# Performance work log

Hardware: AMD Instinct MI355X
Metric: run time of the kernel (lower is better)

## Reference

```python
import jax, jax.numpy as jnp
import numpy as np

TEMP = 1.0
EPS = 1e-8


def setup_inputs() -> dict:
    key = jax.random.key(0)
    k1, k2 = jax.random.split(key)
    x = jax.random.normal(k1, (8, 2048, 128), dtype=jnp.float32)
    codebook = jax.random.normal(k2, (8192, 128), dtype=jnp.float32)
    return {"x": x, "codebook": codebook}


def reference(x, codebook):
    # dim = -1: feature axis already last, moveaxis is identity.
    batch_shape = x.shape[:-1]
    xf = x.reshape(-1, x.shape[-1])  # [N, D]
    # Euclidean cdist via ||a-b||^2 = ||a||^2 + ||b||^2 - 2 a.b
    x2 = jnp.sum(xf * xf, axis=-1, keepdims=True)        # [N, 1]
    c2 = jnp.sum(codebook * codebook, axis=-1)           # [V]
    d2 = x2 + c2 - 2.0 * (xf @ codebook.T)               # [N, V]
    dists = jnp.sqrt(jnp.maximum(d2, 0.0))
    idxes = jnp.argmin(dists, axis=-1)                   # [N]
    # softmax(log(d + eps) * temp) == normalized d^temp (distance-weighted attention)
    attn = jax.nn.softmax(jnp.log(dists + EPS) * TEMP, axis=-1)  # [N, V]
    embed = attn @ codebook                              # [N, D]
    embed = embed.reshape(*batch_shape, -1)
    idxes = idxes.reshape(batch_shape)
    return embed, idxes
```

## Files before the change

### kernel.cpp

```cpp
#include <hip/hip_runtime.h>
#include <stdint.h>

#define NROWS 16384
#define DIM   128
#define VOCAB 8192
#define BN 64
#define BV 64
#define VSPLITS 4
#define SPLITV (VOCAB / VSPLITS)
#define NTILES (SPLITV / BV)
#define MARGIN  0.8f
#define EMB_ELEMS (NROWS * DIM)
#define LIST_CAP_MAX 4194304u
#define LCAP 512

typedef __attribute__((ext_vector_type(8))) short bf16x8;
typedef __attribute__((ext_vector_type(4))) float f32x4;

__device__ __forceinline__ unsigned short f2bf(float f) {
  union { float f; unsigned u; } v; v.f = f;
  unsigned r = v.u + 0x7fffu + ((v.u >> 16) & 1u);
  return (unsigned short)(r >> 16);
}

__device__ __forceinline__ int cvt_pk_bf16(float lo, float hi) {
  int r;
  asm("v_cvt_pk_bf16_f32 %0, %1, %2" : "=v"(r) : "v"(lo), "v"(hi));
  return r;
}

__device__ __forceinline__ bf16x8 pack8(float4 a, float4 b) {
  bf16x8 r;
  r[0] = (short)f2bf(a.x); r[1] = (short)f2bf(a.y);
  r[2] = (short)f2bf(a.z); r[3] = (short)f2bf(a.w);
  r[4] = (short)f2bf(b.x); r[5] = (short)f2bf(b.y);
  r[6] = (short)f2bf(b.z); r[7] = (short)f2bf(b.w);
  return r;
}

__global__ __launch_bounds__(256) void k_prep(const float* __restrict__ cb,
                                              float* __restrict__ c2,
                                              unsigned short* __restrict__ cbf) {
  int tid = threadIdx.x;
  int r = blockIdx.x * 16 + (tid >> 4);
  int l = tid & 15;
  const float* rp = cb + (size_t)r * DIM + l * 8;
  float4 a = *(const float4*)rp;
  float4 b = *(const float4*)(rp + 4);
  float s = a.x*a.x + a.y*a.y + a.z*a.z + a.w*a.w
          + b.x*b.x + b.y*b.y + b.z*b.z + b.w*b.w;
  bf16x8 v8 = pack8(a, b);
  *(bf16x8*)(cbf + (size_t)r * DIM + l * 8) = v8;
#pragma unroll
  for (int o = 1; o < 16; o <<= 1) s += __shfl_xor(s, o);
  if (l == 0) c2[r] = s;
}

__global__ __launch_bounds__(256, 4) void k_main(
    const float* __restrict__ x, const float* __restrict__ c2g,
    const unsigned short* __restrict__ cbf,
    float* __restrict__ accum,
    unsigned int* __restrict__ cnt,
    unsigned int* __restrict__ list, unsigned int cap) {
  __shared__ unsigned short tile1[BV][136];
  __shared__ unsigned short tileT[DIM][72];
  __shared__ unsigned int lbuf[LCAP];
  __shared__ unsigned int lcnt;
  __shared__ unsigned int gbase;

  const int tid = threadIdx.x;
  const int lane = tid & 63;
  const int w = tid >> 6;
  const int l15 = lane & 15, lq = lane >> 4;
  const int blockRow = blockIdx.x * BN;
  const int vy = blockIdx.y;

  if (tid == 0) lcnt = 0;

  bf16x8 afrag[4];
  float x2 = 0.f;
  {
    int gr = blockRow + w * 16 + l15;
    const float* xr = x + (size_t)gr * DIM + lq * 8;
#pragma unroll
    for (int kf = 0; kf < 4; ++kf) {
      float4 a = *(const float4*)(xr + kf * 32);
      float4 b = *(const float4*)(xr + kf * 32 + 4);
      x2 += a.x*a.x + a.y*a.y + a.z*a.z + a.w*a.w
          + b.x*b.x + b.y*b.y + b.z*b.z + b.w*b.w;
      afrag[kf] = pack8(a, b);
    }
    x2 += __shfl_xor(x2, 16);
    x2 += __shfl_xor(x2, 32);
  }

  f32x4 eacc[8];
#pragma unroll
  for (int db = 0; db < 8; ++db) eacc[db] = (f32x4){0.f, 0.f, 0.f, 0.f};
  float den = 0.f;
  float runminD = 3.0e19f;

  const int sv = (tid >> 4) * 4;
  const int sd = (tid & 15) * 8;
  const int sS = (tid & 7) << 4;

  const int srcA = (l15 + ((lane & 16) << 1)) << 2;
  const int srcB = srcA + 64;

  for (int it = 0; it < NTILES; ++it) {
    int vbase = vy * SPLITV + it * BV;
    __syncthreads();
    {
      uint4 r0 = *(const uint4*)(cbf + (size_t)(vbase + sv + 0) * DIM + sd);
      uint4 r1 = *(const uint4*)(cbf + (size_t)(vbase + sv + 1) * DIM + sd);
      uint4 r2 = *(const uint4*)(cbf + (size_t)(vbase + sv + 2) * DIM + sd);
      uint4 r3 = *(const uint4*)(cbf + (size_t)(vbase + sv + 3) * DIM + sd);
      *(uint4*)&tile1[sv + 0][sd] = r0;
      *(uint4*)&tile1[sv + 1][sd] = r1;
      *(uint4*)&tile1[sv + 2][sd] = r2;
      *(uint4*)&tile1[sv + 3][sd] = r3;
      const unsigned short* s0 = (const unsigned short*)&r0;
      const unsigned short* s1 = (const unsigned short*)&r1;
      const unsigned short* s2 = (const unsigned short*)&r2;
      const unsigned short* s3 = (const unsigned short*)&r3;
      char* tb = (char*)&tileT[0][0];
#pragma unroll
      for (int k = 0; k < 8; ++k) {
        uint2 val;
        val.x = (unsigned)s0[k] | ((unsigned)s1[k] << 16);
        val.y = (unsigned)s2[k] | ((unsigned)s3[k] << 16);
        *(uint2*)(tb + (sd + k) * 144 + ((sv * 2) ^ sS)) = val;
      }
    }
    float4 c2v0 = *(const float4*)(c2g + vbase + 0 * 16 + lq * 4);
    float4 c2v1 = *(const float4*)(c2g + vbase + 1 * 16 + lq * 4);
    float4 c2v2 = *(const float4*)(c2g + vbase + 2 * 16 + lq * 4);
    float4 c2v3 = *(const float4*)(c2g + vbase + 3 * 16 + lq * 4);
    __syncthreads();
    f32x4 sacc[4];
#pragma unroll
    for (int vi = 0; vi < 4; ++vi) sacc[vi] = (f32x4){0.f, 0.f, 0.f, 0.f};
#pragma unroll
    for (int kf = 0; kf < 4; ++kf) {
#pragma unroll
      for (int vi = 0; vi < 4; ++vi) {
        bf16x8 cf = *(const bf16x8*)&tile1[vi * 16 + l15][kf * 32 + lq * 8];
        sacc[vi] = __builtin_amdgcn_mfma_f32_16x16x32_bf16(cf, afrag[kf], sacc[vi], 0, 0, 0);
      }
    }
    float dd[4][4];
    const float* c2p[4] = {&c2v0.x, &c2v1.x, &c2v2.x, &c2v3.x};
#pragma unroll
    for (int vi = 0; vi < 4; ++vi)
#pragma unroll
      for (int j = 0; j < 4; ++j) {
        float d2 = fmaxf(fmaf(-2.f, sacc[vi][j], x2 + c2p[vi][j]), 0.f);
        float dist = sqrtf(d2) + 1e-8f;
        dd[vi][j] = dist;
        den += dist;
      }
    float rm = dd[0][0];
#pragma unroll
    for (int vi = 0; vi < 4; ++vi)
#pragma unroll
      for (int j = 0; j < 4; ++j) rm = fminf(rm, dd[vi][j]);
    rm = fminf(rm, __shfl_xor(rm, 16));
    rm = fminf(rm, __shfl_xor(rm, 32));
    runminD = fminf(runminD, rm);
    float thrD = sqrtf(fmaf(runminD, runminD, MARGIN)) + 2e-8f;
    if (__any(rm <= thrD)) {
      unsigned grow = (unsigned)(blockRow + w * 16 + l15);
#pragma unroll
      for (int vi = 0; vi < 4; ++vi)
#pragma unroll
        for (int j = 0; j < 4; ++j) {
          if (dd[vi][j] <= thrD) {
            unsigned gv = (unsigned)(vbase + vi * 16 + lq * 4 + j);
            unsigned ent = (grow << 13) | gv;
            unsigned pos = atomicAdd(&lcnt, 1u);
            if (pos < LCAP) {
              lbuf[pos] = ent;
            } else {
              unsigned gp = atomicAdd(cnt, 1u);
              if (gp < cap) list[gp] = ent;
            }
          }
        }
    }
    int wlo[4], whi[4];
#pragma unroll
    for (int vi = 0; vi < 4; ++vi) {
      wlo[vi] = cvt_pk_bf16(dd[vi][0], dd[vi][1]);
      whi[vi] = cvt_pk_bf16(dd[vi][2], dd[vi][3]);
    }
    const char* tb = (const char*)&tileT[0][0];
#pragma unroll
    for (int ks = 0; ks < 2; ++ks) {
      int v0 = ks * 2, v1 = ks * 2 + 1;
      int t0, t1;
      union { int u[4]; bf16x8 v8; } A;
      t0 = __builtin_amdgcn_ds_bpermute(srcA, wlo[v0]);
      t1 = __builtin_amdgcn_ds_bpermute(srcA, wlo[v1]);
      A.u[0] = (lq & 2) ? t1 : t0;
      t0 = __builtin_amdgcn_ds_bpermute(srcA, whi[v0]);
      t1 = __builtin_amdgcn_ds_bpermute(srcA, whi[v1]);
      A.u[1] = (lq & 2) ? t1 : t0;
      t0 = __builtin_amdgcn_ds_bpermute(srcB, wlo[v0]);
      t1 = __builtin_amdgcn_ds_bpermute(srcB, wlo[v1]);
      A.u[2] = (lq & 2) ? t1 : t0;
      t0 = __builtin_amdgcn_ds_bpermute(srcB, whi[v0]);
      t1 = __builtin_amdgcn_ds_bpermute(srcB, whi[v1]);
      A.u[3] = (lq & 2) ? t1 : t0;
      int voff = (ks * 32 + lq * 8) * 2;
#pragma unroll
      for (int db = 0; db < 8; ++db) {
        int d = db * 16 + l15;
        bf16x8 bw = *(const bf16x8*)(tb + d * 144 + (voff ^ (((d >> 3) & 7) << 4)));
        eacc[db] = __builtin_amdgcn_mfma_f32_16x16x32_bf16(A.v8, bw, eacc[db], 0, 0, 0);
      }
    }
  }
  __syncthreads();
  unsigned total = lcnt < LCAP ? lcnt : LCAP;
  if (tid == 0) gbase = atomicAdd(cnt, total);
  __syncthreads();
  for (unsigned i = tid; i < total; i += 256) {
    unsigned p = gbase + i;
    if (p < cap) list[p] = lbuf[i];
  }
#pragma unroll
  for (int db = 0; db < 8; ++db) {
#pragma unroll
    for (int j = 0; j < 4; ++j) {
      int grow = blockRow + w * 16 + lq * 4 + j;
      atomicAdd(&accum[(size_t)grow * 129 + db * 16 + l15], eacc[db][j]);
    }
  }
  den += __shfl_xor(den, 16);
  den += __shfl_xor(den, 32);
  if (lq == 0)
    atomicAdd(&accum[(size_t)(blockRow + w * 16 + l15) * 129 + 128], den);
}

__global__ __launch_bounds__(256) void k_fix(const float* __restrict__ x,
                                             const float* __restrict__ cb,
                                             const unsigned int* __restrict__ list,
                                             const unsigned int* __restrict__ cnt,
                                             unsigned int cap,
                                             unsigned long long* __restrict__ kExact) {
  unsigned n = *cnt; if (n > cap) n = cap;
  int lane = threadIdx.x & 63;
  unsigned wave = blockIdx.x * (blockDim.x >> 6) + (threadIdx.x >> 6);
  unsigned nw = gridDim.x * (blockDim.x >> 6);
  for (unsigned e = wave; e < n; e += nw) {
    unsigned ent = list[e];
    unsigned row = ent >> 13;
    unsigned v = ent & 0x1FFFu;
    const float* xr = x + (size_t)row * DIM;
    const float* cr = cb + (size_t)v * DIM;
    float2 xa = *(const float2*)(xr + lane * 2);
    float2 ca = *(const float2*)(cr + lane * 2);
    double d0 = (double)xa.x - (double)ca.x;
    double d1 = (double)xa.y - (double)ca.y;
    double acc = d0 * d0 + d1 * d1;
    for (int off = 32; off; off >>= 1) acc += __shfl_down(acc, off);
    if (lane == 0)
      atomicMin(&kExact[row],
                ((unsigned long long)__float_as_uint((float)acc) << 32) | (unsigned long long)v);
  }
}

__global__ __launch_bounds__(256) void k_rescue(const float* __restrict__ x,
                                                const float* __restrict__ cb,
                                                const unsigned int* __restrict__ cnt,
                                                unsigned int cap,
                                                unsigned long long* __restrict__ kExact) {
  if (*cnt <= cap) return;
  __shared__ float xs[4][128];
  int lane = threadIdx.x & 63;
  int wv = threadIdx.x >> 6;
  int row = blockIdx.x * 4 + wv;
  float2 xa = *(const float2*)(x + (size_t)row * DIM + lane * 2);
  xs[wv][lane * 2] = xa.x;
  xs[wv][lane * 2 + 1] = xa.y;
  __syncthreads();
  unsigned long long best = ~0ull;
  for (int v0 = 0; v0 < VOCAB; v0 += 64) {
    int v = v0 + lane;
    const float* cr = cb + (size_t)v * DIM;
    double acc = 0.0;
    for (int d = 0; d < DIM; ++d) {
      double diff = (double)xs[wv][d] - (double)cr[d];
      acc = fma(diff, diff, acc);
    }
    unsigned long long p = ((unsigned long long)__float_as_uint((float)acc) << 32)
                         | (unsigned long long)(unsigned)v;
    best = (p < best) ? p : best;
  }
#pragma unroll
  for (int off = 32; off; off >>= 1) {
    unsigned long long o = __shfl_xor(best, off);
    best = (o < best) ? o : best;
  }
  if (lane == 0) atomicMin(&kExact[row], best);
}

__global__ __launch_bounds__(256) void k_out(const float* __restrict__ accum,
                                             const unsigned long long* __restrict__ kExact,
                                             float* __restrict__ out) {
  int i = blockIdx.x * 256 + threadIdx.x;
  if (i < EMB_ELEMS) {
    int row = i >> 7, d = i & 127;
    float s = accum[(size_t)row * 129 + 128];
    out[i] = accum[(size_t)row * 129 + d] / s;
  } else {
    int n = i - EMB_ELEMS;
    out[EMB_ELEMS + n] = (float)(unsigned)(kExact[n] & 0x1FFFu);
  }
}

extern "C" void kernel_launch(void* const* d_in, const int* in_sizes, int n_in,
                              void* d_out, int out_size, void* d_ws, size_t ws_size,
                              hipStream_t stream) {
  const float* x = (const float*)d_in[0];
  const float* cb = (const float*)d_in[1];
  float* out = (float*)d_out;

  char* ws = (char*)d_ws;
  size_t off = 0;
  float* accum = (float*)(ws + off); off += (size_t)NROWS * 129 * 4;
  float* c2 = (float*)(ws + off); off += (size_t)VOCAB * 4;
  unsigned short* cbf = (unsigned short*)(ws + off); off += (size_t)VOCAB * DIM * 2;
  unsigned long long* kExact = (unsigned long long*)(ws + off); off += (size_t)NROWS * 8;
  unsigned int* cnt = (unsigned int*)(ws + off); off += 64;
  unsigned int* list = (unsigned int*)(ws + off);
  size_t cap32 = (ws_size > off) ? (ws_size - off) / 4 : 0;
  unsigned cap = (unsigned)(cap32 > LIST_CAP_MAX ? LIST_CAP_MAX : cap32);

  hipMemsetAsync(accum, 0, (size_t)NROWS * 129 * 4, stream);
  hipMemsetAsync(kExact, 0xFF, (size_t)NROWS * 8, stream);
  hipMemsetAsync(cnt, 0, 64, stream);

  k_prep<<<VOCAB / 16, 256, 0, stream>>>(cb, c2, cbf);
  k_main<<<dim3(NROWS / BN, VSPLITS), 256, 0, stream>>>(x, c2, cbf, accum, cnt, list, cap);
  k_fix<<<1024, 256, 0, stream>>>(x, cb, list, cnt, cap, kExact);
  k_rescue<<<NROWS / 4, 256, 0, stream>>>(x, cb, cnt, cap, kExact);
  k_out<<<(EMB_ELEMS + NROWS) / 256, 256, 0, stream>>>(accum, kExact, out);
}
```

Baseline: 329.7 us.

## Switch main kernel to 32x32 MFMA with global codebook fragments and pre-transposed copy

Rewrites the main distance/attention kernel to use 32x32x16 bf16 MFMA tiles with 128-row blocks and 8 vocab splits. The LDS staging and barriers are dropped: codebook fragments come straight from global/L2, and a new k_tr kernel builds a transposed bf16 codebook so the second matmul can also read directly. The distance accumulator is reused as the A operand via v_permlane32_swap instead of ds_bpermute shuffles. This removes the LDS transpose and sync cost but relies on cache hits for repeated codebook reads and raises register pressure.

```diff
diff --git a/kernel.cpp b/kernel.cpp
--- a/kernel.cpp
+++ b/kernel.cpp
@@ -4,9 +4,9 @@
 #define NROWS 16384
 #define DIM   128
 #define VOCAB 8192
-#define BN 64
+#define BN 128
 #define BV 64
-#define VSPLITS 4
+#define VSPLITS 8
 #define SPLITV (VOCAB / VSPLITS)
 #define NTILES (SPLITV / BV)
 #define MARGIN  0.8f
@@ -16,6 +16,7 @@
 
 typedef __attribute__((ext_vector_type(8))) short bf16x8;
 typedef __attribute__((ext_vector_type(4))) float f32x4;
+typedef __attribute__((ext_vector_type(16))) float f32x16;
 
 __device__ __forceinline__ unsigned short f2bf(float f) {
   union { float f; unsigned u; } v; v.f = f;
@@ -27,6 +28,10 @@
   int r;
   asm("v_cvt_pk_bf16_f32 %0, %1, %2" : "=v"(r) : "v"(lo), "v"(hi));
   return r;
+}
+
+__device__ __forceinline__ void permlane_swap(int& a, int& b) {
+  asm("v_permlane32_swap_b32 %0, %1" : "+v"(a), "+v"(b));
 }
 
 __device__ __forceinline__ bf16x8 pack8(float4 a, float4 b) {
@@ -56,14 +61,36 @@
   if (l == 0) c2[r] = s;
 }
 
-__global__ __launch_bounds__(256, 4) void k_main(
+__global__ __launch_bounds__(256) void k_tr(const unsigned short* __restrict__ cbf,
+                                            unsigned short* __restrict__ cbfT) {
+  __shared__ unsigned short t[64][72];
+  int vb = blockIdx.x * 64, db = blockIdx.y * 64;
+  int tid = threadIdx.x;
+#pragma unroll
+  for (int ph = 0; ph < 2; ++ph) {
+    int r = (tid >> 3) + ph * 32;
+    int c = (tid & 7) * 8;
+    *(uint4*)&t[r][c] = *(const uint4*)(cbf + (size_t)(vb + r) * DIM + db + c);
+  }
+  __syncthreads();
+#pragma unroll
+  for (int ph = 0; ph < 2; ++ph) {
+    int d = (tid >> 3) + ph * 32;
+    int v8 = (tid & 7) * 8;
+    union { uint4 u4; unsigned short s[8]; } val;
+#pragma unroll
+    for (int k = 0; k < 8; ++k) val.s[k] = t[v8 + k][d];
+    *(uint4*)(cbfT + (size_t)(db + d) * VOCAB + vb + v8) = val.u4;
+  }
+}
+
+__global__ __launch_bounds__(256, 3) void k_main(
     const float* __restrict__ x, const float* __restrict__ c2g,
     const unsigned short* __restrict__ cbf,
+    const unsigned short* __restrict__ cbfT,
     float* __restrict__ accum,
     unsigned int* __restrict__ cnt,
     unsigned int* __restrict__ list, unsigned int cap) {
-  __shared__ unsigned short tile1[BV][136];
-  __shared__ unsigned short tileT[DIM][72];
   __shared__ unsigned int lbuf[LCAP];
   __shared__ unsigned int lcnt;
   __shared__ unsigned int gbase;
@@ -71,111 +98,81 @@
   const int tid = threadIdx.x;
   const int lane = tid & 63;
   const int w = tid >> 6;
-  const int l15 = lane & 15, lq = lane >> 4;
+  const int l31 = lane & 31, h = lane >> 5;
   const int blockRow = blockIdx.x * BN;
   const int vy = blockIdx.y;
 
   if (tid == 0) lcnt = 0;
 
-  bf16x8 afrag[4];
+  bf16x8 afrag[8];
   float x2 = 0.f;
   {
-    int gr = blockRow + w * 16 + l15;
-    const float* xr = x + (size_t)gr * DIM + lq * 8;
-#pragma unroll
-    for (int kf = 0; kf < 4; ++kf) {
-      float4 a = *(const float4*)(xr + kf * 32);
-      float4 b = *(const float4*)(xr + kf * 32 + 4);
+    int gr = blockRow + w * 32 + l31;
+    const float* xr = x + (size_t)gr * DIM + h * 8;
+#pragma unroll
+    for (int ks = 0; ks < 8; ++ks) {
+      float4 a = *(const float4*)(xr + ks * 16);
+      float4 b = *(const float4*)(xr + ks * 16 + 4);
       x2 += a.x*a.x + a.y*a.y + a.z*a.z + a.w*a.w
           + b.x*b.x + b.y*b.y + b.z*b.z + b.w*b.w;
-      afrag[kf] = pack8(a, b);
-    }
-    x2 += __shfl_xor(x2, 16);
+      afrag[ks] = pack8(a, b);
+    }
     x2 += __shfl_xor(x2, 32);
   }
 
-  f32x4 eacc[8];
-#pragma unroll
-  for (int db = 0; db < 8; ++db) eacc[db] = (f32x4){0.f, 0.f, 0.f, 0.f};
+  f32x16 eacc[4];
+#pragma unroll
+  for (int db = 0; db < 4; ++db)
+#pragma unroll
+    for (int i = 0; i < 16; ++i) eacc[db][i] = 0.f;
   float den = 0.f;
   float runminD = 3.0e19f;
 
-  const int sv = (tid >> 4) * 4;
-  const int sd = (tid & 15) * 8;
-  const int sS = (tid & 7) << 4;
-
-  const int srcA = (l15 + ((lane & 16) << 1)) << 2;
-  const int srcB = srcA + 64;
-
   for (int it = 0; it < NTILES; ++it) {
-    int vbase = vy * SPLITV + it * BV;
-    __syncthreads();
-    {
-      uint4 r0 = *(const uint4*)(cbf + (size_t)(vbase + sv + 0) * DIM + sd);
-      uint4 r1 = *(const uint4*)(cbf + (size_t)(vbase + sv + 1) * DIM + sd);
-      uint4 r2 = *(const uint4*)(cbf + (size_t)(vbase + sv + 2) * DIM + sd);
-      uint4 r3 = *(const uint4*)(cbf + (size_t)(vbase + sv + 3) * DIM + sd);
-      *(uint4*)&tile1[sv + 0][sd] = r0;
-      *(uint4*)&tile1[sv + 1][sd] = r1;
-      *(uint4*)&tile1[sv + 2][sd] = r2;
-      *(uint4*)&tile1[sv + 3][sd] = r3;
-      const unsigned short* s0 = (const unsigned short*)&r0;
-      const unsigned short* s1 = (const unsigned short*)&r1;
-      const unsigned short* s2 = (const unsigned short*)&r2;
-      const unsigned short* s3 = (const unsigned short*)&r3;
-      char* tb = (char*)&tileT[0][0];
-#pragma unroll
-      for (int k = 0; k < 8; ++k) {
-        uint2 val;
-        val.x = (unsigned)s0[k] | ((unsigned)s1[k] << 16);
-        val.y = (unsigned)s2[k] | ((unsigned)s3[k] << 16);
-        *(uint2*)(tb + (sd + k) * 144 + ((sv * 2) ^ sS)) = val;
+    const int vbase = vy * SPLITV + it * BV;
+    f32x16 sacc[2];
+#pragma unroll
+    for (int vblk = 0; vblk < 2; ++vblk) {
+#pragma unroll
+      for (int i = 0; i < 16; ++i) sacc[vblk][i] = 0.f;
+      const unsigned short* arow = cbf + (size_t)(vbase + vblk * 32 + l31) * DIM + h * 8;
+#pragma unroll
+      for (int ks = 0; ks < 8; ++ks) {
+        bf16x8 cf = *(const bf16x8*)(arow + ks * 16);
+        sacc[vblk] = __builtin_amdgcn_mfma_f32_32x32x16_bf16(cf, afrag[ks], sacc[vblk], 0, 0, 0);
       }
     }
-    float4 c2v0 = *(const float4*)(c2g + vbase + 0 * 16 + lq * 4);
-    float4 c2v1 = *(const float4*)(c2g + vbase + 1 * 16 + lq * 4);
-    float4 c2v2 = *(const float4*)(c2g + vbase + 2 * 16 + lq * 4);
-    float4 c2v3 = *(const float4*)(c2g + vbase + 3 * 16 + lq * 4);
-    __syncthreads();
-    f32x4 sacc[4];
-#pragma unroll
-    for (int vi = 0; vi < 4; ++vi) sacc[vi] = (f32x4){0.f, 0.f, 0.f, 0.f};
-#pragma unroll
-    for (int kf = 0; kf < 4; ++kf) {
-#pragma unroll
-      for (int vi = 0; vi < 4; ++vi) {
-        bf16x8 cf = *(const bf16x8*)&tile1[vi * 16 + l15][kf * 32 + lq * 8];
-        sacc[vi] = __builtin_amdgcn_mfma_f32_16x16x32_bf16(cf, afrag[kf], sacc[vi], 0, 0, 0);
+#pragma unroll
+    for (int vblk = 0; vblk < 2; ++vblk) {
+#pragma unroll
+      for (int g = 0; g < 4; ++g) {
+        f32x4 c2f = *(const f32x4*)(c2g + vbase + vblk * 32 + g * 8 + h * 4);
+#pragma unroll
+        for (int q = 0; q < 4; ++q) {
+          int r = g * 4 + q;
+          float d2 = fmaxf(fmaf(-2.f, sacc[vblk][r], x2 + c2f[q]), 0.f);
+          float dist = sqrtf(d2) + 1e-8f;
+          den += dist;
+          sacc[vblk][r] = dist;
+        }
       }
     }
-    float dd[4][4];
-    const float* c2p[4] = {&c2v0.x, &c2v1.x, &c2v2.x, &c2v3.x};
-#pragma unroll
-    for (int vi = 0; vi < 4; ++vi)
-#pragma unroll
-      for (int j = 0; j < 4; ++j) {
-        float d2 = fmaxf(fmaf(-2.f, sacc[vi][j], x2 + c2p[vi][j]), 0.f);
-        float dist = sqrtf(d2) + 1e-8f;
-        dd[vi][j] = dist;
-        den += dist;
-      }
-    float rm = dd[0][0];
-#pragma unroll
-    for (int vi = 0; vi < 4; ++vi)
-#pragma unroll
-      for (int j = 0; j < 4; ++j) rm = fminf(rm, dd[vi][j]);
-    rm = fminf(rm, __shfl_xor(rm, 16));
+    float rm = sacc[0][0];
+#pragma unroll
+    for (int vblk = 0; vblk < 2; ++vblk)
+#pragma unroll
+      for (int r = 0; r < 16; ++r) rm = fminf(rm, sacc[vblk][r]);
     rm = fminf(rm, __shfl_xor(rm, 32));
     runminD = fminf(runminD, rm);
     float thrD = sqrtf(fmaf(runminD, runminD, MARGIN)) + 2e-8f;
     if (__any(rm <= thrD)) {
-      unsigned grow = (unsigned)(blockRow + w * 16 + l15);
-#pragma unroll
-      for (int vi = 0; vi < 4; ++vi)
-#pragma unroll
-        for (int j = 0; j < 4; ++j) {
-          if (dd[vi][j] <= thrD) {
-            unsigned gv = (unsigned)(vbase + vi * 16 + lq * 4 + j);
+      unsigned grow = (unsigned)(blockRow + w * 32 + l31);
+#pragma unroll
+      for (int vblk = 0; vblk < 2; ++vblk)
+#pragma unroll
+        for (int r = 0; r < 16; ++r) {
+          if (sacc[vblk][r] <= thrD) {
+            unsigned gv = (unsigned)(vbase + vblk * 32 + (r & 3) + 8 * (r >> 2) + 4 * h);
             unsigned ent = (grow << 13) | gv;
             unsigned pos = atomicAdd(&lcnt, 1u);
             if (pos < LCAP) {
@@ -187,36 +184,32 @@
           }
         }
     }
-    int wlo[4], whi[4];
-#pragma unroll
-    for (int vi = 0; vi < 4; ++vi) {
-      wlo[vi] = cvt_pk_bf16(dd[vi][0], dd[vi][1]);
-      whi[vi] = cvt_pk_bf16(dd[vi][2], dd[vi][3]);
-    }
-    const char* tb = (const char*)&tileT[0][0];
-#pragma unroll
-    for (int ks = 0; ks < 2; ++ks) {
-      int v0 = ks * 2, v1 = ks * 2 + 1;
-      int t0, t1;
-      union { int u[4]; bf16x8 v8; } A;
-      t0 = __builtin_amdgcn_ds_bpermute(srcA, wlo[v0]);
-      t1 = __builtin_amdgcn_ds_bpermute(srcA, wlo[v1]);
-      A.u[0] = (lq & 2) ? t1 : t0;
-      t0 = __builtin_amdgcn_ds_bpermute(srcA, whi[v0]);
-      t1 = __builtin_amdgcn_ds_bpermute(srcA, whi[v1]);
-      A.u[1] = (lq & 2) ? t1 : t0;
-      t0 = __builtin_amdgcn_ds_bpermute(srcB, wlo[v0]);
-      t1 = __builtin_amdgcn_ds_bpermute(srcB, wlo[v1]);
-      A.u[2] = (lq & 2) ? t1 : t0;
-      t0 = __builtin_amdgcn_ds_bpermute(srcB, whi[v0]);
-      t1 = __builtin_amdgcn_ds_bpermute(srcB, whi[v1]);
-      A.u[3] = (lq & 2) ? t1 : t0;
-      int voff = (ks * 32 + lq * 8) * 2;
-#pragma unroll
-      for (int db = 0; db < 8; ++db) {
-        int d = db * 16 + l15;
-        bf16x8 bw = *(const bf16x8*)(tb + d * 144 + (voff ^ (((d >> 3) & 7) << 4)));
-        eacc[db] = __builtin_amdgcn_mfma_f32_16x16x32_bf16(A.v8, bw, eacc[db], 0, 0, 0);
+#pragma unroll
+    for (int vblk = 0; vblk < 2; ++vblk) {
+      int p0 = cvt_pk_bf16(sacc[vblk][0],  sacc[vblk][1]);
+      int p1 = cvt_pk_bf16(sacc[vblk][2],  sacc[vblk][3]);
+      int p2 = cvt_pk_bf16(sacc[vblk][4],  sacc[vblk][5]);
+      int p3 = cvt_pk_bf16(sacc[vblk][6],  sacc[vblk][7]);
+      int p4 = cvt_pk_bf16(sacc[vblk][8],  sacc[vblk][9]);
+      int p5 = cvt_pk_bf16(sacc[vblk][10], sacc[vblk][11]);
+      int p6 = cvt_pk_bf16(sacc[vblk][12], sacc[vblk][13]);
+      int p7 = cvt_pk_bf16(sacc[vblk][14], sacc[vblk][15]);
+      permlane_swap(p0, p2);
+      permlane_swap(p1, p3);
+      permlane_swap(p4, p6);
+      permlane_swap(p5, p7);
+#pragma unroll
+      for (int t = 0; t < 2; ++t) {
+        union { int u[4]; bf16x8 v8; } A;
+        A.u[0] = t ? p4 : p0; A.u[1] = t ? p5 : p1;
+        A.u[2] = t ? p6 : p2; A.u[3] = t ? p7 : p3;
+        int ks = vblk * 2 + t;
+        const unsigned short* bcol = cbfT + (size_t)vbase + ks * 16 + h * 8;
+#pragma unroll
+        for (int dblk = 0; dblk < 4; ++dblk) {
+          bf16x8 bw = *(const bf16x8*)(bcol + (size_t)(dblk * 32 + l31) * VOCAB);
+          eacc[dblk] = __builtin_amdgcn_mfma_f32_32x32x16_bf16(A.v8, bw, eacc[dblk], 0, 0, 0);
+        }
       }
     }
   }
@@ -229,17 +222,16 @@
     if (p < cap) list[p] = lbuf[i];
   }
 #pragma unroll
-  for (int db = 0; db < 8; ++db) {
-#pragma unroll
-    for (int j = 0; j < 4; ++j) {
-      int grow = blockRow + w * 16 + lq * 4 + j;
-      atomicAdd(&accum[(size_t)grow * 129 + db * 16 + l15], eacc[db][j]);
-    }
-  }
-  den += __shfl_xor(den, 16);
+  for (int dblk = 0; dblk < 4; ++dblk) {
+#pragma unroll
+    for (int r = 0; r < 16; ++r) {
+      int grow = blockRow + w * 32 + (r & 3) + 8 * (r >> 2) + 4 * h;
+      atomicAdd(&accum[(size_t)grow * 129 + dblk * 32 + l31], eacc[dblk][r]);
+    }
+  }
   den += __shfl_xor(den, 32);
-  if (lq == 0)
-    atomicAdd(&accum[(size_t)(blockRow + w * 16 + l15) * 129 + 128], den);
+  if (h == 0)
+    atomicAdd(&accum[(size_t)(blockRow + w * 32 + l31) * 129 + 128], den);
 }
 
 __global__ __launch_bounds__(256) void k_fix(const float* __restrict__ x,
@@ -331,6 +323,7 @@
   float* accum = (float*)(ws + off); off += (size_t)NROWS * 129 * 4;
   float* c2 = (float*)(ws + off); off += (size_t)VOCAB * 4;
   unsigned short* cbf = (unsigned short*)(ws + off); off += (size_t)VOCAB * DIM * 2;
+  unsigned short* cbfT = (unsigned short*)(ws + off); off += (size_t)VOCAB * DIM * 2;
   unsigned long long* kExact = (unsigned long long*)(ws + off); off += (size_t)NROWS * 8;
   unsigned int* cnt = (unsigned int*)(ws + off); off += 64;
   unsigned int* list = (unsigned int*)(ws + off);
@@ -342,7 +335,8 @@
   hipMemsetAsync(cnt, 0, 64, stream);
 
   k_prep<<<VOCAB / 16, 256, 0, stream>>>(cb, c2, cbf);
-  k_main<<<dim3(NROWS / BN, VSPLITS), 256, 0, stream>>>(x, c2, cbf, accum, cnt, list, cap);
+  k_tr<<<dim3(VOCAB / 64, DIM / 64), 256, 0, stream>>>(cbf, cbfT);
+  k_main<<<dim3(NROWS / BN, VSPLITS), 256, 0, stream>>>(x, c2, cbf, cbfT, accum, cnt, list, cap);
   k_fix<<<1024, 256, 0, stream>>>(x, cb, list, cnt, cap, kExact);
   k_rescue<<<NROWS / 4, 256, 0, stream>>>(x, cb, cnt, cap, kExact);
   k_out<<<(EMB_ELEMS + NROWS) / 256, 256, 0, stream>>>(accum, kExact, out);
```

New measurement: 592.2 us. 1.8x slower.
